# Kernel optimization log

Hardware: AMD Instinct MI355X
Metric: run time of the kernel (lower is better)

## Reference

```python
import jax, jax.numpy as jnp
import numpy as np

B, T, I, H = 512, 49, 96, 1024  # batch, input_window_size-1, 3*nbones, hidden


def setup_inputs() -> dict:
    key = jax.random.key(0)
    k1, k2, k3, k4, k5 = jax.random.split(key, 5)
    s = 1.0 / np.sqrt(H)  # torch GRUCell init scale
    return {
        "enc_in": jax.random.normal(k1, (B, T, I), dtype=jnp.float32),
        "W_ih": jax.random.uniform(k2, (3 * H, I), jnp.float32, -s, s),
        "W_hh": jax.random.uniform(k3, (3 * H, H), jnp.float32, -s, s),
        "b_ih": jax.random.uniform(k4, (3 * H,), jnp.float32, -s, s),
        "b_hh": jax.random.uniform(k5, (3 * H,), jnp.float32, -s, s),
        "train": 1,
    }


def reference(enc_in, W_ih, W_hh, b_ih, b_hh, train):
    # Precompute input projections for all timesteps: [T, B, 3H]
    gi = jnp.einsum("bti,gi->tbg", enc_in, W_ih) + b_ih
    hdim = W_hh.shape[1]

    def step(h, gi_t):
        gh = h @ W_hh.T + b_hh                      # [B, 3H]
        ir, iz, inn = jnp.split(gi_t, 3, axis=-1)   # torch gate order: r, z, n
        hr, hz, hn = jnp.split(gh, 3, axis=-1)
        r = jax.nn.sigmoid(ir + hr)
        z = jax.nn.sigmoid(iz + hz)
        n = jnp.tanh(inn + r * hn)
        h_new = (1.0 - z) * n + z * h
        return h_new, None

    h0 = jnp.zeros((enc_in.shape[0], hdim), dtype=enc_in.dtype)
    h_last, _ = jax.lax.scan(step, h0, gi)
    return h_last  # enc_state: [B, H]
```

## Files before the change

### kernel.cpp

```cpp
#include <hip/hip_runtime.h>
#include <hip/hip_bf16.h>

#define B_ 512
#define T_ 49
#define I_ 96
#define H_ 1024

typedef __attribute__((ext_vector_type(4))) float f32x4;
typedef __attribute__((ext_vector_type(8))) short s16x8;

__device__ __forceinline__ unsigned short f2bf(float f) {
    unsigned int u = __float_as_uint(f);
    unsigned int r = (u + 0x7FFFu + ((u >> 16) & 1u)) >> 16;
    return (unsigned short)r;
}
__device__ __forceinline__ float sigmoidf_(float x) {
    return 1.0f / (1.0f + __expf(-x));
}
__device__ __forceinline__ float tanhf_(float x) {
    return 1.0f - 2.0f / (__expf(2.0f * x) + 1.0f);
}

__global__ void quantize_kernel(const float* __restrict__ Whh,
                                const float* __restrict__ Wih,
                                const float* __restrict__ x,
                                unsigned short* __restrict__ Whh_bf,
                                unsigned short* __restrict__ Wih_bf,
                                unsigned short* __restrict__ xT_bf) {
    const long stride = (long)gridDim.x * blockDim.x;
    const long idx = (long)blockIdx.x * blockDim.x + threadIdx.x;

    const long nWhh4 = (long)3 * H_ * H_ / 4;
    const long nWih4 = (long)3 * H_ * I_ / 4;
    const long nX4   = (long)B_ * T_ * I_ / 4;

    for (long i = idx; i < nWhh4; i += stride) {
        float4 v = ((const float4*)Whh)[i];
        ushort4 o; o.x = f2bf(v.x); o.y = f2bf(v.y); o.z = f2bf(v.z); o.w = f2bf(v.w);
        ((ushort4*)Whh_bf)[i] = o;
    }
    for (long i = idx; i < nWih4; i += stride) {
        float4 v = ((const float4*)Wih)[i];
        ushort4 o; o.x = f2bf(v.x); o.y = f2bf(v.y); o.z = f2bf(v.z); o.w = f2bf(v.w);
        ((ushort4*)Wih_bf)[i] = o;
    }
    for (long i = idx; i < nX4; i += stride) {
        float4 v = ((const float4*)x)[i];
        ushort4 o; o.x = f2bf(v.x); o.y = f2bf(v.y); o.z = f2bf(v.z); o.w = f2bf(v.w);
        const long e = i * 4;
        const int b  = (int)(e / (T_ * I_));
        const int rm = (int)(e - (long)b * (T_ * I_));
        const int tt = rm / I_;
        const int ii = rm - tt * I_;
        ((ushort4*)xT_bf)[(((long)tt * B_ + b) * I_ + ii) >> 2] = o;
    }
}

__global__ __launch_bounds__(512)
void gru_step2(const unsigned short* __restrict__ Whh_bf,
               const unsigned short* __restrict__ Wih_bf,
               const unsigned short* __restrict__ xT_bf,
               const float* __restrict__ b_ih,
               const float* __restrict__ b_hh,
               const float* __restrict__ h_in,
               const unsigned short* __restrict__ hbf_in,
               float* __restrict__ h_out,
               unsigned short* __restrict__ hbf_out,
               int t, int first)
{
    const int tid = threadIdx.x;
    const int w   = tid >> 6;
    const int l   = tid & 63;
    const int l15 = l & 15;
    const int l4  = l >> 4;

    const int bid  = blockIdx.x;
    const int xcd  = bid & 7;
    const int r_   = bid >> 3;
    const int blkb = r_ & 3;
    const int blkj = xcd * 8 + (r_ >> 2);
    const int b0   = blkb * 128;
    const int j0   = blkj * 16;
    const int wb   = b0 + w * 16;

    __shared__ __align__(16) unsigned short Wl[2][3][16][264];

    f32x4 aR  = (f32x4){0.f, 0.f, 0.f, 0.f};
    f32x4 aZ  = (f32x4){0.f, 0.f, 0.f, 0.f};
    f32x4 aNi = (f32x4){0.f, 0.f, 0.f, 0.f};
    f32x4 aNh = (f32x4){0.f, 0.f, 0.f, 0.f};

    const int jj = tid >> 5;
    const int ch = tid & 31;
    s16x8 sw0, sw1, sw2;

#define WSTAGE_LOAD(c) {                                                       \
    const long ko = (long)(c) * 256 + ch * 8;                                  \
    sw0 = *(const s16x8*)(Whh_bf + ((long)(           j0 + jj)) * H_ + ko);    \
    sw1 = *(const s16x8*)(Whh_bf + ((long)(H_     +   j0 + jj)) * H_ + ko);    \
    sw2 = *(const s16x8*)(Whh_bf + ((long)(2 * H_ +   j0 + jj)) * H_ + ko); }

#define WSTAGE_WRITE(buf) {                                                    \
    *(s16x8*)&Wl[buf][0][jj][ch * 8] = sw0;                                    \
    *(s16x8*)&Wl[buf][1][jj][ch * 8] = sw1;                                    \
    *(s16x8*)&Wl[buf][2][jj][ch * 8] = sw2; }

    const unsigned short* Abase = hbf_in + (long)(wb + l15) * H_ + l4 * 8;
    s16x8 Acur[8];
    float hp[4] = {0.f, 0.f, 0.f, 0.f};
    const int jg = j0 + l15;

    if (!first) {
        WSTAGE_LOAD(0);
#pragma unroll
        for (int q = 0; q < 8; ++q)
            Acur[q] = *(const s16x8*)(Abase + q * 32);
#pragma unroll
        for (int r = 0; r < 4; ++r)
            hp[r] = h_in[(long)(wb + l4 * 4 + r) * H_ + jg];
    }

    {
        const unsigned short* Ax = xT_bf + ((long)t * B_ + (wb + l15)) * I_ + l4 * 8;
        const unsigned short* Vr = Wih_bf + (long)(j0 + l15) * I_ + l4 * 8;
        const unsigned short* Vz = Wih_bf + (long)(H_ + j0 + l15) * I_ + l4 * 8;
        const unsigned short* Vn = Wih_bf + (long)(2 * H_ + j0 + l15) * I_ + l4 * 8;
#pragma unroll
        for (int ks = 0; ks < 3; ++ks) {
            s16x8 a  = *(const s16x8*)(Ax + ks * 32);
            s16x8 br = *(const s16x8*)(Vr + ks * 32);
            s16x8 bz = *(const s16x8*)(Vz + ks * 32);
            s16x8 bn = *(const s16x8*)(Vn + ks * 32);
            aR  = __builtin_amdgcn_mfma_f32_16x16x32_bf16(a, br, aR, 0, 0, 0);
            aZ  = __builtin_amdgcn_mfma_f32_16x16x32_bf16(a, bz, aZ, 0, 0, 0);
            aNi = __builtin_amdgcn_mfma_f32_16x16x32_bf16(a, bn, aNi, 0, 0, 0);
        }
    }

    if (!first) {
        WSTAGE_WRITE(0);
        __syncthreads();
#pragma unroll
        for (int c = 0; c < 4; ++c) {
            s16x8 An[8];
            if (c < 3) {
                WSTAGE_LOAD(c + 1);
#pragma unroll
                for (int q = 0; q < 8; ++q)
                    An[q] = *(const s16x8*)(Abase + ((c + 1) * 8 + q) * 32);
            }
#pragma unroll
            for (int q = 0; q < 8; ++q) {
                s16x8 br = *(const s16x8*)&Wl[c & 1][0][l15][q * 32 + l4 * 8];
                s16x8 bz = *(const s16x8*)&Wl[c & 1][1][l15][q * 32 + l4 * 8];
                s16x8 bn = *(const s16x8*)&Wl[c & 1][2][l15][q * 32 + l4 * 8];
                aR  = __builtin_amdgcn_mfma_f32_16x16x32_bf16(Acur[q], br, aR, 0, 0, 0);
                aZ  = __builtin_amdgcn_mfma_f32_16x16x32_bf16(Acur[q], bz, aZ, 0, 0, 0);
                aNh = __builtin_amdgcn_mfma_f32_16x16x32_bf16(Acur[q], bn, aNh, 0, 0, 0);
            }
            if (c < 3) {
                WSTAGE_WRITE((c & 1) ^ 1);
                __syncthreads();
#pragma unroll
                for (int q = 0; q < 8; ++q) Acur[q] = An[q];
            }
        }
    }
#undef WSTAGE_LOAD
#undef WSTAGE_WRITE

    const float bR   = b_ih[jg] + b_hh[jg];
    const float bZ   = b_ih[H_ + jg] + b_hh[H_ + jg];
    const float bihN = b_ih[2 * H_ + jg];
    const float bhhN = b_hh[2 * H_ + jg];

#pragma unroll
    for (int r = 0; r < 4; ++r) {
        const int row = wb + l4 * 4 + r;
        const long off = (long)row * H_ + jg;
        const float rg = sigmoidf_(aR[r] + bR);
        const float zg = sigmoidf_(aZ[r] + bZ);
        const float ng = tanhf_(aNi[r] + bihN + rg * (aNh[r] + bhhN));
        const float hn = (1.0f - zg) * ng + zg * hp[r];
        h_out[off] = hn;
        hbf_out[off] = f2bf(hn);
    }
}

extern "C" void kernel_launch(void* const* d_in, const int* in_sizes, int n_in,
                              void* d_out, int out_size, void* d_ws, size_t ws_size,
                              hipStream_t stream) {
    const float* enc_in = (const float*)d_in[0];
    const float* W_ih   = (const float*)d_in[1];
    const float* W_hh   = (const float*)d_in[2];
    const float* b_ih   = (const float*)d_in[3];
    const float* b_hh   = (const float*)d_in[4];
    float* out = (float*)d_out;

    char* ws = (char*)d_ws;
    unsigned short* Whh_bf = (unsigned short*)(ws);
    unsigned short* Wih_bf = (unsigned short*)(ws + 6291456);
    unsigned short* xT_bf  = (unsigned short*)(ws + 6881280);
    float* hA              = (float*)(ws + 11698176);
    float* hB              = (float*)(ws + 13795328);
    unsigned short* hbfA   = (unsigned short*)(ws + 15892480);
    unsigned short* hbfB   = (unsigned short*)(ws + 16941056);

    quantize_kernel<<<dim3(1024), dim3(256), 0, stream>>>(W_hh, W_ih, enc_in,
                                                          Whh_bf, Wih_bf, xT_bf);

    for (int t = 0; t < T_; ++t) {
        const int first = (t == 0) ? 1 : 0;
        float* hi; unsigned short* hbi; float* ho; unsigned short* hbo;
        if (t & 1) { hi = hA; hbi = hbfA; ho = hB; hbo = hbfB; }
        else       { hi = hB; hbi = hbfB; ho = hA; hbo = hbfA; }
        if (t == T_ - 1) ho = out;
        gru_step2<<<dim3(256), dim3(512), 0, stream>>>(Whh_bf, Wih_bf, xT_bf,
                                                       b_ih, b_hh, hi, hbi, ho, hbo,
                                                       t, first);
    }
}
```

Measured before the change: 664.8 us.

## Load whole W_hh tile via direct global-to-LDS and split K across waves

Each block now loads its full 3x16x1024 W_hh slice into swizzled LDS at once with global_load_lds, replacing the double-buffered register-staged loop and its repeated barriers. Waves are arranged as 4 batch groups × 2 K halves, each wave computing two 16-row M tiles so every LDS weight fragment feeds two MFMAs. Partial sums from the two K halves are combined through an LDS reduction buffer before the gate epilogue. This uses much more LDS per block (roughly 128 KB) and adds a reduction step and extra barriers.

After: 734.3 us. +10.5%, slower.

```diff
diff --git a/kernel.cpp b/kernel.cpp
--- a/kernel.cpp
+++ b/kernel.cpp
@@ -19,6 +19,12 @@
 }
 __device__ __forceinline__ float tanhf_(float x) {
     return 1.0f - 2.0f / (__expf(2.0f * x) + 1.0f);
+}
+
+__device__ __forceinline__ void gload_lds16(const unsigned short* g, unsigned short* l) {
+    __builtin_amdgcn_global_load_lds(
+        (const __attribute__((address_space(1))) void*)g,
+        (__attribute__((address_space(3))) void*)l, 16, 0, 0);
 }
 
 __global__ void quantize_kernel(const float* __restrict__ Whh,
@@ -57,7 +63,7 @@
 }
 
 __global__ __launch_bounds__(512)
-void gru_step2(const unsigned short* __restrict__ Whh_bf,
+void gru_step3(const unsigned short* __restrict__ Whh_bf,
                const unsigned short* __restrict__ Wih_bf,
                const unsigned short* __restrict__ xT_bf,
                const float* __restrict__ b_ih,
@@ -68,11 +74,16 @@
                unsigned short* __restrict__ hbf_out,
                int t, int first)
 {
+    __shared__ __align__(16) unsigned short Wl[3 * 16 * 1024];
+    __shared__ __align__(16) f32x4 Red[4 * 8 * 64];
+
     const int tid = threadIdx.x;
     const int w   = tid >> 6;
     const int l   = tid & 63;
     const int l15 = l & 15;
     const int l4  = l >> 4;
+    const int mq  = w >> 1;
+    const int kg  = w & 1;
 
     const int bid  = blockIdx.x;
     const int xcd  = bid & 7;
@@ -81,109 +92,149 @@
     const int blkj = xcd * 8 + (r_ >> 2);
     const int b0   = blkb * 128;
     const int j0   = blkj * 16;
-    const int wb   = b0 + w * 16;
-
-    __shared__ __align__(16) unsigned short Wl[2][3][16][264];
-
-    f32x4 aR  = (f32x4){0.f, 0.f, 0.f, 0.f};
-    f32x4 aZ  = (f32x4){0.f, 0.f, 0.f, 0.f};
-    f32x4 aNi = (f32x4){0.f, 0.f, 0.f, 0.f};
-    f32x4 aNh = (f32x4){0.f, 0.f, 0.f, 0.f};
-
-    const int jj = tid >> 5;
-    const int ch = tid & 31;
-    s16x8 sw0, sw1, sw2;
-
-#define WSTAGE_LOAD(c) {                                                       \
-    const long ko = (long)(c) * 256 + ch * 8;                                  \
-    sw0 = *(const s16x8*)(Whh_bf + ((long)(           j0 + jj)) * H_ + ko);    \
-    sw1 = *(const s16x8*)(Whh_bf + ((long)(H_     +   j0 + jj)) * H_ + ko);    \
-    sw2 = *(const s16x8*)(Whh_bf + ((long)(2 * H_ +   j0 + jj)) * H_ + ko); }
-
-#define WSTAGE_WRITE(buf) {                                                    \
-    *(s16x8*)&Wl[buf][0][jj][ch * 8] = sw0;                                    \
-    *(s16x8*)&Wl[buf][1][jj][ch * 8] = sw1;                                    \
-    *(s16x8*)&Wl[buf][2][jj][ch * 8] = sw2; }
-
-    const unsigned short* Abase = hbf_in + (long)(wb + l15) * H_ + l4 * 8;
-    s16x8 Acur[8];
-    float hp[4] = {0.f, 0.f, 0.f, 0.f};
-    const int jg = j0 + l15;
+    const int jg   = j0 + l15;
+    const int brow = b0 + mq * 32;
 
     if (!first) {
-        WSTAGE_LOAD(0);
-#pragma unroll
-        for (int q = 0; q < 8; ++q)
-            Acur[q] = *(const s16x8*)(Abase + q * 32);
-#pragma unroll
-        for (int r = 0; r < 4; ++r)
-            hp[r] = h_in[(long)(wb + l4 * 4 + r) * H_ + jg];
-    }
-
-    {
-        const unsigned short* Ax = xT_bf + ((long)t * B_ + (wb + l15)) * I_ + l4 * 8;
-        const unsigned short* Vr = Wih_bf + (long)(j0 + l15) * I_ + l4 * 8;
-        const unsigned short* Vz = Wih_bf + (long)(H_ + j0 + l15) * I_ + l4 * 8;
-        const unsigned short* Vn = Wih_bf + (long)(2 * H_ + j0 + l15) * I_ + l4 * 8;
+#pragma unroll
+        for (int i = 0; i < 12; ++i) {
+            const int row  = w * 6 + (i >> 1);
+            const int half = i & 1;
+            const int g    = row >> 4;
+            const int jj   = row & 15;
+            const unsigned short* src = Whh_bf
+                + ((long)g * H_ + j0 + jj) * H_ + half * 512
+                + ((l ^ (jj & 7)) * 8);
+            unsigned short* dst = Wl + (g * 16 + jj) * 1024 + half * 512;
+            gload_lds16(src, dst);
+        }
+    }
+
+    f32x4 accR[2], accZ[2], accNh[2], accNi[2];
+#pragma unroll
+    for (int m = 0; m < 2; ++m) {
+        accR[m]  = (f32x4){0.f, 0.f, 0.f, 0.f};
+        accZ[m]  = (f32x4){0.f, 0.f, 0.f, 0.f};
+        accNh[m] = (f32x4){0.f, 0.f, 0.f, 0.f};
+        accNi[m] = (f32x4){0.f, 0.f, 0.f, 0.f};
+    }
+
+    float hp[2][4] = {{0.f,0.f,0.f,0.f},{0.f,0.f,0.f,0.f}};
+    if (kg == 0 && !first) {
+#pragma unroll
+        for (int f = 0; f < 2; ++f)
+#pragma unroll
+            for (int r = 0; r < 4; ++r)
+                hp[f][r] = h_in[(long)(brow + f * 16 + l4 * 4 + r) * H_ + jg];
+    }
+
+    if (kg == 1) {
+        const unsigned short* Ax0 = xT_bf + ((long)t * B_ + brow + l15) * I_ + l4 * 8;
+        const unsigned short* Ax1 = Ax0 + 16 * I_;
+        const unsigned short* Vr  = Wih_bf + (long)(j0 + l15) * I_ + l4 * 8;
+        const unsigned short* Vz  = Wih_bf + (long)(H_ + j0 + l15) * I_ + l4 * 8;
+        const unsigned short* Vn  = Wih_bf + (long)(2 * H_ + j0 + l15) * I_ + l4 * 8;
 #pragma unroll
         for (int ks = 0; ks < 3; ++ks) {
-            s16x8 a  = *(const s16x8*)(Ax + ks * 32);
+            s16x8 a0 = *(const s16x8*)(Ax0 + ks * 32);
+            s16x8 a1 = *(const s16x8*)(Ax1 + ks * 32);
             s16x8 br = *(const s16x8*)(Vr + ks * 32);
             s16x8 bz = *(const s16x8*)(Vz + ks * 32);
             s16x8 bn = *(const s16x8*)(Vn + ks * 32);
-            aR  = __builtin_amdgcn_mfma_f32_16x16x32_bf16(a, br, aR, 0, 0, 0);
-            aZ  = __builtin_amdgcn_mfma_f32_16x16x32_bf16(a, bz, aZ, 0, 0, 0);
-            aNi = __builtin_amdgcn_mfma_f32_16x16x32_bf16(a, bn, aNi, 0, 0, 0);
+            accR[0]  = __builtin_amdgcn_mfma_f32_16x16x32_bf16(a0, br, accR[0], 0, 0, 0);
+            accR[1]  = __builtin_amdgcn_mfma_f32_16x16x32_bf16(a1, br, accR[1], 0, 0, 0);
+            accZ[0]  = __builtin_amdgcn_mfma_f32_16x16x32_bf16(a0, bz, accZ[0], 0, 0, 0);
+            accZ[1]  = __builtin_amdgcn_mfma_f32_16x16x32_bf16(a1, bz, accZ[1], 0, 0, 0);
+            accNi[0] = __builtin_amdgcn_mfma_f32_16x16x32_bf16(a0, bn, accNi[0], 0, 0, 0);
+            accNi[1] = __builtin_amdgcn_mfma_f32_16x16x32_bf16(a1, bn, accNi[1], 0, 0, 0);
         }
     }
 
     if (!first) {
-        WSTAGE_WRITE(0);
+        const unsigned short* Ab0 = hbf_in + (long)(brow + l15) * H_ + kg * 512 + l4 * 8;
+        const unsigned short* Ab1 = Ab0 + 16 * H_;
+        const unsigned short* Wr  = Wl + (0 * 16 + l15) * 1024;
+        const unsigned short* Wz  = Wl + (1 * 16 + l15) * 1024;
+        const unsigned short* Wn  = Wl + (2 * 16 + l15) * 1024;
+        const int swz   = (l15 & 7) << 3;
+        const int kbase = kg * 512 + l4 * 8;
+
+        s16x8 ring[3][4];
+
+#pragma unroll
+        for (int p = 0; p < 2; ++p) {
+            ring[p][0] = *(const s16x8*)(Ab0 + p * 64);
+            ring[p][1] = *(const s16x8*)(Ab0 + p * 64 + 32);
+            ring[p][2] = *(const s16x8*)(Ab1 + p * 64);
+            ring[p][3] = *(const s16x8*)(Ab1 + p * 64 + 32);
+        }
+
         __syncthreads();
-#pragma unroll
-        for (int c = 0; c < 4; ++c) {
-            s16x8 An[8];
-            if (c < 3) {
-                WSTAGE_LOAD(c + 1);
-#pragma unroll
-                for (int q = 0; q < 8; ++q)
-                    An[q] = *(const s16x8*)(Abase + ((c + 1) * 8 + q) * 32);
+
+#pragma unroll
+        for (int kk = 0; kk < 8; ++kk) {
+            const int cur = kk % 3;
+            const int nxt = (kk + 2) % 3;
+            if (kk < 6) {
+                ring[nxt][0] = *(const s16x8*)(Ab0 + (kk + 2) * 64);
+                ring[nxt][1] = *(const s16x8*)(Ab0 + (kk + 2) * 64 + 32);
+                ring[nxt][2] = *(const s16x8*)(Ab1 + (kk + 2) * 64);
+                ring[nxt][3] = *(const s16x8*)(Ab1 + (kk + 2) * 64 + 32);
             }
 #pragma unroll
-            for (int q = 0; q < 8; ++q) {
-                s16x8 br = *(const s16x8*)&Wl[c & 1][0][l15][q * 32 + l4 * 8];
-                s16x8 bz = *(const s16x8*)&Wl[c & 1][1][l15][q * 32 + l4 * 8];
-                s16x8 bn = *(const s16x8*)&Wl[c & 1][2][l15][q * 32 + l4 * 8];
-                aR  = __builtin_amdgcn_mfma_f32_16x16x32_bf16(Acur[q], br, aR, 0, 0, 0);
-                aZ  = __builtin_amdgcn_mfma_f32_16x16x32_bf16(Acur[q], bz, aZ, 0, 0, 0);
-                aNh = __builtin_amdgcn_mfma_f32_16x16x32_bf16(Acur[q], bn, aNh, 0, 0, 0);
+            for (int q = 0; q < 2; ++q) {
+                const int off = ((kbase + (kk * 2 + q) * 32) ^ swz);
+                s16x8 br = *(const s16x8*)(Wr + off);
+                s16x8 bz = *(const s16x8*)(Wz + off);
+                s16x8 bn = *(const s16x8*)(Wn + off);
+                s16x8 a0 = ring[cur][q * 1 + 0];
+                s16x8 a1 = ring[cur][q * 1 + 2];
+                accR[0]  = __builtin_amdgcn_mfma_f32_16x16x32_bf16(a0, br, accR[0], 0, 0, 0);
+                accR[1]  = __builtin_amdgcn_mfma_f32_16x16x32_bf16(a1, br, accR[1], 0, 0, 0);
+                accZ[0]  = __builtin_amdgcn_mfma_f32_16x16x32_bf16(a0, bz, accZ[0], 0, 0, 0);
+                accZ[1]  = __builtin_amdgcn_mfma_f32_16x16x32_bf16(a1, bz, accZ[1], 0, 0, 0);
+                accNh[0] = __builtin_amdgcn_mfma_f32_16x16x32_bf16(a0, bn, accNh[0], 0, 0, 0);
+                accNh[1] = __builtin_amdgcn_mfma_f32_16x16x32_bf16(a1, bn, accNh[1], 0, 0, 0);
             }
-            if (c < 3) {
-                WSTAGE_WRITE((c & 1) ^ 1);
-                __syncthreads();
-#pragma unroll
-                for (int q = 0; q < 8; ++q) Acur[q] = An[q];
+        }
+    }
+
+    __syncthreads();
+    if (kg == 1) {
+        f32x4* dst = &Red[(mq * 8) * 64 + l];
+        dst[0 * 64] = accR[0];  dst[1 * 64] = accR[1];
+        dst[2 * 64] = accZ[0];  dst[3 * 64] = accZ[1];
+        dst[4 * 64] = accNh[0]; dst[5 * 64] = accNh[1];
+        dst[6 * 64] = accNi[0]; dst[7 * 64] = accNi[1];
+    }
+    __syncthreads();
+
+    if (kg == 0) {
+        const f32x4* srcp = &Red[(mq * 8) * 64 + l];
+        accR[0]  += srcp[0 * 64]; accR[1]  += srcp[1 * 64];
+        accZ[0]  += srcp[2 * 64]; accZ[1]  += srcp[3 * 64];
+        accNh[0] += srcp[4 * 64]; accNh[1] += srcp[5 * 64];
+        accNi[0] += srcp[6 * 64]; accNi[1] += srcp[7 * 64];
+
+        const float bR   = b_ih[jg] + b_hh[jg];
+        const float bZ   = b_ih[H_ + jg] + b_hh[H_ + jg];
+        const float bihN = b_ih[2 * H_ + jg];
+        const float bhhN = b_hh[2 * H_ + jg];
+
+#pragma unroll
+        for (int f = 0; f < 2; ++f) {
+#pragma unroll
+            for (int r = 0; r < 4; ++r) {
+                const int row = brow + f * 16 + l4 * 4 + r;
+                const long off = (long)row * H_ + jg;
+                const float rg = sigmoidf_(accR[f][r] + bR);
+                const float zg = sigmoidf_(accZ[f][r] + bZ);
+                const float ng = tanhf_(accNi[f][r] + bihN + rg * (accNh[f][r] + bhhN));
+                const float hn = (1.0f - zg) * ng + zg * hp[f][r];
+                h_out[off] = hn;
+                hbf_out[off] = f2bf(hn);
             }
         }
-    }
-#undef WSTAGE_LOAD
-#undef WSTAGE_WRITE
-
-    const float bR   = b_ih[jg] + b_hh[jg];
-    const float bZ   = b_ih[H_ + jg] + b_hh[H_ + jg];
-    const float bihN = b_ih[2 * H_ + jg];
-    const float bhhN = b_hh[2 * H_ + jg];
-
-#pragma unroll
-    for (int r = 0; r < 4; ++r) {
-        const int row = wb + l4 * 4 + r;
-        const long off = (long)row * H_ + jg;
-        const float rg = sigmoidf_(aR[r] + bR);
-        const float zg = sigmoidf_(aZ[r] + bZ);
-        const float ng = tanhf_(aNi[r] + bihN + rg * (aNh[r] + bhhN));
-        const float hn = (1.0f - zg) * ng + zg * hp[r];
-        h_out[off] = hn;
-        hbf_out[off] = f2bf(hn);
     }
 }
 
@@ -215,7 +266,7 @@
         if (t & 1) { hi = hA; hbi = hbfA; ho = hB; hbo = hbfB; }
         else       { hi = hB; hbi = hbfB; ho = hA; hbo = hbfA; }
         if (t == T_ - 1) ho = out;
-        gru_step2<<<dim3(256), dim3(512), 0, stream>>>(Whh_bf, Wih_bf, xT_bf,
+        gru_step3<<<dim3(256), dim3(512), 0, stream>>>(Whh_bf, Wih_bf, xT_bf,
                                                        b_ih, b_hh, hi, hbi, ho, hbo,
                                                        t, first);
     }
```
